# Optimization experiments

Hardware: AMD Instinct MI355X
Metric: run time of the kernel (lower is better)

## Reference

```python
import jax, jax.numpy as jnp
import numpy as np
import math

N_WAY, K_SHOT, Q_QUERY, PRJ_NUM, D = 5, 5, 15, 6, 64


def setup_inputs() -> dict:
    key = jax.random.key(0)
    k1, k2 = jax.random.split(key)
    feat = jax.random.normal(k1, (600, 64, 10, 10), dtype=jnp.float32)
    label = jax.random.randint(k2, (450,), 0, N_WAY)
    scale = jnp.ones((1,), dtype=jnp.float32)
    r = jnp.zeros((2,), dtype=jnp.float32)
    return {"feat": feat, "label": label, "scale": scale, "r": r}


def reference(feat, label, scale, r):
    ns = N_WAY * K_SHOT * PRJ_NUM  # 150 support images
    inv_sqrt_d = 1.0 / math.sqrt(D)
    support_xf = feat[:ns] * inv_sqrt_d
    query_xf = feat[ns:] * inv_sqrt_d
    q, c, h, w = query_xf.shape

    # support: (n_way, k_shot*prj_num*h*w, c)
    support = support_xf.reshape(N_WAY, K_SHOT * PRJ_NUM, c, h * w)
    support = jnp.transpose(support, (0, 1, 3, 2)).reshape(N_WAY, -1, c)
    # query: (q*h*w, c)
    query = jnp.transpose(query_xf.reshape(q, c, h * w), (0, 2, 1)).reshape(q * h * w, c)

    alpha, beta = r[0], r[1]
    reg = support.shape[1] / support.shape[2]
    lam = reg * jnp.exp(alpha)
    rho = jnp.exp(beta)

    # Woodbury / normal-equations path: hat = (S^T S + lam I)^-1 S^T S, per class
    sts = jnp.einsum('nkc,nkd->ncd', support, support)  # (n_way, c, c)
    m = sts + lam * jnp.eye(c, dtype=sts.dtype)[None]
    hat = jnp.linalg.inv(m) @ sts  # (n_way, c, c)

    Q_bar = jnp.einsum('qc,ncd->nqd', query, hat) * rho  # (n_way, q*h*w, c)
    dist = jnp.sum((Q_bar - query[None]) ** 2, axis=2).T  # (q*h*w, n_way)
    neg_l2_dist = -dist.reshape(q, h * w, N_WAY).mean(axis=1)  # (q, n_way)

    y_pred = jax.nn.softmax(neg_l2_dist, axis=1)
    logits = neg_l2_dist * scale[0]
    logp = jax.nn.log_softmax(logits, axis=1)
    loss = -jnp.mean(jnp.take_along_axis(logp, label[:, None], axis=1))
    return y_pred, loss
```

## Files before the change

kernel.cpp:

```cpp
#include <hip/hip_runtime.h>
#include <math.h>


typedef __attribute__((ext_vector_type(8))) short short8;
typedef __attribute__((ext_vector_type(4))) short short4v;
typedef __attribute__((ext_vector_type(4))) float f32x4;

#define NSUP 150
#define NQ 450
#define PIX 100
#define IMG_STRIDE 6400
#define MAGIC 0x5F3D2B1Cu

static __device__ __forceinline__ short bf16r(float x) {
  unsigned u = __builtin_bit_cast(unsigned, x);
  u += 0x7FFFu + ((u >> 16) & 1u);
  return (short)(u >> 16);
}
static __device__ __forceinline__ float b2f(short v) {
  return __builtin_bit_cast(float, ((unsigned)(unsigned short)v) << 16);
}
static __device__ __forceinline__ void st_flag(unsigned* p, unsigned v) {
  __builtin_amdgcn_fence(__ATOMIC_RELEASE, "agent");
  __hip_atomic_store(p, v, __ATOMIC_RELAXED, __HIP_MEMORY_SCOPE_AGENT);
}
static __device__ __forceinline__ void spin_rlx(unsigned* p) {
  int guard = 1 << 22;
  while (__hip_atomic_load(p, __ATOMIC_RELAXED, __HIP_MEMORY_SCOPE_AGENT) != MAGIC
         && --guard) __builtin_amdgcn_s_sleep(2);
}

static __device__ __forceinline__ void gram_accum(const float* __restrict__ f,
                                                  f32x4 acc[4][4], int r, int g) {
  #pragma unroll
  for (int ks = 0; ks < 4; ++ks) {
    short8 frag[4];
    const int kb = ks * 32 + g * 8;
    #pragma unroll
    for (int R = 0; R < 4; ++R) {
      short8 q;
      const float* p = f + (R * 16 + r) * PIX + kb;
      if (ks < 3) {
        float4 lo = *(const float4*)p;
        float4 hi = *(const float4*)(p + 4);
        q[0] = bf16r(lo.x); q[1] = bf16r(lo.y); q[2] = bf16r(lo.z); q[3] = bf16r(lo.w);
        q[4] = bf16r(hi.x); q[5] = bf16r(hi.y); q[6] = bf16r(hi.z); q[7] = bf16r(hi.w);
      } else if (g == 0) {
        float4 lo = *(const float4*)p;
        q[0] = bf16r(lo.x); q[1] = bf16r(lo.y); q[2] = bf16r(lo.z); q[3] = bf16r(lo.w);
        q[4] = 0; q[5] = 0; q[6] = 0; q[7] = 0;
      } else {
        #pragma unroll
        for (int j = 0; j < 8; ++j) q[j] = 0;
      }
      frag[R] = q;
    }
    #pragma unroll
    for (int R = 0; R < 4; ++R)
      #pragma unroll
      for (int C = 0; C < 4; ++C)
        acc[R][C] = __builtin_amdgcn_mfma_f32_16x16x32_bf16(frag[R], frag[C],
                                                            acc[R][C], 0, 0, 0);
  }
}

static __device__ __forceinline__ void mm64q(const short* A, const short* B,
                                             f32x4 t[2][2], int r, int g,
                                             int wr, int wc) {
  #pragma unroll
  for (int ks = 0; ks < 2; ++ks) {
    short8 af[2], bfr[2];
    #pragma unroll
    for (int i = 0; i < 2; ++i) {
      af[i]  = *(const short8*)(A + (wr * 32 + i * 16 + r) * 72 + ks * 32 + g * 8);
      bfr[i] = *(const short8*)(B + (wc * 32 + i * 16 + r) * 72 + ks * 32 + g * 8);
    }
    #pragma unroll
    for (int i = 0; i < 2; ++i)
      #pragma unroll
      for (int j = 0; j < 2; ++j)
        t[i][j] = __builtin_amdgcn_mfma_f32_16x16x32_bf16(af[i], bfr[j],
                                                          t[i][j], 0, 0, 0);
  }
}

#define ZERO_ACC4(t)                                  \
  _Pragma("unroll") for (int R = 0; R < 4; ++R)       \
  _Pragma("unroll") for (int C = 0; C < 4; ++C)       \
  _Pragma("unroll") for (int q = 0; q < 4; ++q) t[R][C][q] = 0.f;

#define ZERO_ACC2(t)                                  \
  _Pragma("unroll") for (int R = 0; R < 2; ++R)       \
  _Pragma("unroll") for (int C = 0; C < 2; ++C)       \
  _Pragma("unroll") for (int q = 0; q < 4; ++q) t[R][C][q] = 0.f;

__global__ __launch_bounds__(256) void k_fused(
    const float* __restrict__ feat, const int* __restrict__ label,
    const float* __restrict__ scale, const float* __restrict__ rvec,
    float* __restrict__ out,
    float* __restrict__ partial,
    unsigned short* __restrict__ Gneg,
    float* __restrict__ blockloss,
    unsigned* __restrict__ gflag,
    unsigned* __restrict__ sflag,
    unsigned* __restrict__ lflag) {
  __shared__ __align__(16) char smem[65536];
  const int b = blockIdx.x, tid = threadIdx.x;
  const int wave = tid >> 6, lane = tid & 63;
  const int r = lane & 15, g = lane >> 4;

  if (b < 30) {
    float (*gbuf)[4096] = (float (*)[4096])smem;
    const int cls = b / 6, jb = b % 6;
    const int ks = wave, kb = ks * 32 + g * 8;
    f32x4 acc[4][4];
    ZERO_ACC4(acc)
    for (int im = 0; im < 5; ++im) {
      const float* f = feat + (size_t)(cls * 30 + jb * 5 + im) * IMG_STRIDE;
      short8 frag[4];
      #pragma unroll
      for (int R = 0; R < 4; ++R) {
        short8 q;
        const float* p = f + (R * 16 + r) * PIX + kb;
        if (ks < 3) {
          float4 lo = *(const float4*)p;
          float4 hi = *(const float4*)(p + 4);
          q[0] = bf16r(lo.x); q[1] = bf16r(lo.y); q[2] = bf16r(lo.z); q[3] = bf16r(lo.w);
          q[4] = bf16r(hi.x); q[5] = bf16r(hi.y); q[6] = bf16r(hi.z); q[7] = bf16r(hi.w);
        } else if (g == 0) {
          float4 lo = *(const float4*)p;
          q[0] = bf16r(lo.x); q[1] = bf16r(lo.y); q[2] = bf16r(lo.z); q[3] = bf16r(lo.w);
          q[4] = 0; q[5] = 0; q[6] = 0; q[7] = 0;
        } else {
          #pragma unroll
          for (int j = 0; j < 8; ++j) q[j] = 0;
        }
        frag[R] = q;
      }
      #pragma unroll
      for (int R = 0; R < 4; ++R)
        #pragma unroll
        for (int C = 0; C < 4; ++C)
          acc[R][C] = __builtin_amdgcn_mfma_f32_16x16x32_bf16(frag[R], frag[C],
                                                              acc[R][C], 0, 0, 0);
    }
    #pragma unroll
    for (int R = 0; R < 4; ++R)
      #pragma unroll
      for (int C = 0; C < 4; ++C)
        #pragma unroll
        for (int q = 0; q < 4; ++q) {
          const int row = R * 16 + g * 4 + q, col = C * 16 + r;
          gbuf[wave][row * 64 + col] = acc[R][C][q];
        }
    __syncthreads();
    float* outp = partial + (size_t)b * 4096;
    for (int c = tid; c < 1024; c += 256) {
      f32x4 s0 = *(const f32x4*)&gbuf[0][4 * c];
      f32x4 s1 = *(const f32x4*)&gbuf[1][4 * c];
      f32x4 s2 = *(const f32x4*)&gbuf[2][4 * c];
      f32x4 s3 = *(const f32x4*)&gbuf[3][4 * c];
      f32x4 s = s0 + s1 + s2 + s3;
      *(float4*)(outp + 4 * c) = *(float4*)&s;
    }
    __syncthreads();
    if (tid == 0) st_flag(&gflag[b], MAGIC);
    if (b >= 5) return;

    float* Ms   = (float*)(smem);
    short* Mb   = (short*)(smem + 16640);
    short* Tb   = (short*)(smem + 25856);
    short* Xa   = (short*)(smem + 35072);
    short* Xc   = (short*)(smem + 44288);
    float* radp = (float*)(smem + 53504);
    float* scal = (float*)(smem + 54528);

    const int n = b;
    const int wr = wave >> 1, wc = wave & 1;
    const float lam = 46.875f * expf(rvec[0]);
    const float rho = expf(rvec[1]);

    if (tid < 6) spin_rlx(&gflag[6 * n + tid]);
    __syncthreads();
    __builtin_amdgcn_fence(__ATOMIC_ACQUIRE, "agent");

    {
      const float* base = partial + (size_t)n * 6 * 4096;
      for (int c = tid; c < 1024; c += 256) {
        float4 s = {0.f, 0.f, 0.f, 0.f};
        #pragma unroll
        for (int p = 0; p < 6; ++p) {
          float4 v = *(const float4*)(base + p * 4096 + 4 * c);
          s.x += v.x; s.y += v.y; s.z += v.z; s.w += v.w;
        }
        const int e = 4 * c, row = e >> 6, col = e & 63;
        Ms[row * 65 + col + 0] = s.x * (1.f / 64.f);
        Ms[row * 65 + col + 1] = s.y * (1.f / 64.f);
        Ms[row * 65 + col + 2] = s.z * (1.f / 64.f);
        Ms[row * 65 + col + 3] = s.w * (1.f / 64.f);
      }
    }
    __syncthreads();
    if (tid < 64) Ms[tid * 65 + tid] += lam;
    __syncthreads();

    {
      const int row = tid & 63, part = tid >> 6;
      float s = 0.f;
      #pragma unroll
      for (int k = 0; k < 16; ++k) s += fabsf(Ms[row * 65 + part * 16 + k]);
      radp[part * 64 + row] = s;
    }
    __syncthreads();
    if (tid < 64) {
      const float diag = Ms[tid * 65 + tid];
      const float rad = radp[tid] + radp[64 + tid] + radp[128 + tid] +
                        radp[192 + tid] - fabsf(diag);
      float lo = diag - rad, hi = diag + rad;
      for (int off = 32; off; off >>= 1) {
        lo = fminf(lo, __shfl_down(lo, off));
        hi = fmaxf(hi, __shfl_down(hi, off));
      }
      if (tid == 0) {
        const float a = fmaxf(lo, lam);
        const float bb = hi;
        const float s = a + bb, d = bb - a;
        scal[0] = s;
        scal[1] = 8.f / (2.f * s * s - d * d);
      }
    }
    __syncthreads();
    const float s0 = scal[0], theta = scal[1];

    for (int e = tid; e < 4096; e += 256) {
      const int i = e >> 6, j = e & 63;
      const float m = Ms[i * 65 + j];
      Mb[i * 72 + j] = bf16r(m);
      Xa[i * 72 + j] = bf16r(theta * (((i == j) ? s0 : 0.f) - m));
    }
    __syncthreads();

    short* x = Xa;
    short* xn = Xc;
    for (int it = 0; it < 2; ++it) {
      {
        f32x4 t[2][2];
        ZERO_ACC2(t)
        mm64q(x, Mb, t, r, g, wr, wc);
        #pragma unroll
        for (int i = 0; i < 2; ++i)
          #pragma unroll
          for (int j = 0; j < 2; ++j)
            #pragma unroll
            for (int q = 0; q < 4; ++q) {
              const int row = wr * 32 + i * 16 + g * 4 + q;
              const int col = wc * 32 + j * 16 + r;
              Tb[row * 72 + col] = bf16r(t[i][j][q]);
            }
      }
      __syncthreads();
      {
        f32x4 t[2][2];
        ZERO_ACC2(t)
        mm64q(Tb, x, t, r, g, wr, wc);
        #pragma unroll
        for (int i = 0; i < 2; ++i)
          #pragma unroll
          for (int j = 0; j < 2; ++j)
            #pragma unroll
            for (int q = 0; q < 4; ++q) {
              const int row = wr * 32 + i * 16 + g * 4 + q;
              const int col = wc * 32 + j * 16 + r;
              const int idx = row * 72 + col;
              xn[idx] = bf16r(2.f * b2f(x[idx]) - t[i][j][q]);
            }
      }
      __syncthreads();
      short* tmp = x; x = xn; xn = tmp;
    }

    for (int e = tid; e < 4096; e += 256) {
      const int i = e >> 6, j = e & 63;
      const float xv = b2f(x[i * 72 + j]);
      Tb[i * 72 + j] = bf16r(((i == j) ? (rho - 1.f) : 0.f) - rho * lam * xv);
    }
    __syncthreads();

    {
      f32x4 t[2][2];
      ZERO_ACC2(t)
      mm64q(Tb, Tb, t, r, g, wr, wc);
      #pragma unroll
      for (int i = 0; i < 2; ++i)
        #pragma unroll
        for (int j = 0; j < 2; ++j)
          #pragma unroll
          for (int q = 0; q < 4; ++q) {
            const int row = wr * 32 + i * 16 + g * 4 + q;
            const int col = wc * 32 + j * 16 + r;
            Gneg[n * 4096 + row * 64 + col] =
                (unsigned short)bf16r(t[i][j][q] * (-0.01f));
          }
    }
    __syncthreads();
    if (tid == 0) st_flag(&sflag[n], MAGIC);
    return;
  }

  const int img = (b - 30) * 4 + wave;
  const bool ok = img < NQ;
  f32x4 acc[4][4];
  ZERO_ACC4(acc)
  if (ok)
    gram_accum(feat + (size_t)(NSUP + img) * IMG_STRIDE, acc, r, g);

  if (tid < 5) spin_rlx(&sflag[tid]);
  __syncthreads();
  __builtin_amdgcn_fence(__ATOMIC_ACQUIRE, "agent");

  unsigned short* Gs = (unsigned short*)smem;
  for (int e = tid; e < 5120; e += 256) {
    const int e4 = e * 4;
    const int nn = e4 >> 12, rem = e4 & 4095, row = rem >> 6, col = rem & 63;
    *(short4v*)&Gs[nn * 4352 + row * 68 + col] = *(const short4v*)&Gneg[e4];
  }
  __syncthreads();

  float myloss = 0.f;
  float nl[5] = {0.f, 0.f, 0.f, 0.f, 0.f};
  if (ok) {
    #pragma unroll
    for (int R = 0; R < 4; ++R)
      #pragma unroll
      for (int C = 0; C < 4; ++C)
        #pragma unroll
        for (int q = 0; q < 4; ++q) {
          const int row = R * 16 + g * 4 + q, col = C * 16 + r;
          const float cv = acc[R][C][q] * (1.f / 64.f);
          const int idx = row * 68 + col;
          #pragma unroll
          for (int nn = 0; nn < 5; ++nn)
            nl[nn] += b2f((short)Gs[nn * 4352 + idx]) * cv;
        }
    #pragma unroll
    for (int nn = 0; nn < 5; ++nn)
      for (int off = 32; off; off >>= 1) nl[nn] += __shfl_down(nl[nn], off);

    if (lane == 0) {
      float mx = nl[0];
      #pragma unroll
      for (int nn = 1; nn < 5; ++nn) mx = fmaxf(mx, nl[nn]);
      float ex[5], se = 0.f;
      #pragma unroll
      for (int nn = 0; nn < 5; ++nn) { ex[nn] = expf(nl[nn] - mx); se += ex[nn]; }
      const float inv = 1.f / se;
      #pragma unroll
      for (int nn = 0; nn < 5; ++nn) out[img * 5 + nn] = ex[nn] * inv;

      const float sc = scale[0];
      float mx2 = nl[0] * sc;
      #pragma unroll
      for (int nn = 1; nn < 5; ++nn) mx2 = fmaxf(mx2, nl[nn] * sc);
      float se2 = 0.f;
      #pragma unroll
      for (int nn = 0; nn < 5; ++nn) se2 += expf(nl[nn] * sc - mx2);
      myloss = mx2 + logf(se2) - nl[label[img]] * sc;
    }
  }

  float* wl = (float*)(smem + 43584);
  if (lane == 0) wl[wave] = ok ? myloss : 0.f;
  __syncthreads();
  if (tid == 0) {
    blockloss[b - 30] = wl[0] + wl[1] + wl[2] + wl[3];
    st_flag(&lflag[b - 30], MAGIC);
  }

  if (b == 30 && wave == 0) {
    for (int i = lane; i < 113; i += 64) spin_rlx(&lflag[i]);
    __builtin_amdgcn_fence(__ATOMIC_ACQUIRE, "agent");
    float s = 0.f;
    for (int i = lane; i < 113; i += 64) s += blockloss[i];
    for (int off = 32; off; off >>= 1) s += __shfl_down(s, off);
    if (lane == 0) out[2250] = s / 450.f;
  }
}

extern "C" void kernel_launch(void* const* d_in, const int* in_sizes, int n_in,
                              void* d_out, int out_size, void* d_ws, size_t ws_size,
                              hipStream_t stream) {
  const float* feat  = (const float*)d_in[0];
  const int*   label = (const int*)d_in[1];
  const float* scale = (const float*)d_in[2];
  const float* rvec  = (const float*)d_in[3];
  float* out = (float*)d_out;

  char* ws = (char*)d_ws;
  float*          partial   = (float*)ws;
  unsigned short* Gneg      = (unsigned short*)(ws + 491520);
  float*          blockloss = (float*)(ws + 532480);
  unsigned*       flags     = (unsigned*)(ws + 532992);
  unsigned* gflag = flags;
  unsigned* sflag = flags + 32;
  unsigned* lflag = flags + 64;

  k_fused<<<dim3(143), dim3(256), 0, stream>>>(feat, label, scale, rvec, out,
                                               partial, Gneg, blockloss,
                                               gflag, sflag, lflag);
}
```

Baseline: 24.40 us.

## Fuse lambda/bf16 staging, unroll Newton-Schulz steps, repad Gs, hoist label/scale loads

Several small changes ship together. The lambda diagonal add and the bf16 conversion of M now happen in the partial-sum reduction loop, which removes one barrier and one pass over shared memory. The two Newton-Schulz iterations are unrolled by hand, and the final residual transform is folded into the last iteration's epilogue, which drops a separate pass and a barrier. The query path loads scale and label before the spin-wait and switches the Gs shared-memory row pitch from 68 to 80 shorts, presumably to change the LDS bank pattern, with loop unroll pragmas added as well. The extra work in the epilogues and the larger LDS footprint could raise register or LDS pressure.

Result: no change. 24.44 us (+0.2%).

```diff
diff --git a/kernel.cpp b/kernel.cpp
--- a/kernel.cpp
+++ b/kernel.cpp
@@ -115,6 +115,7 @@
     const int ks = wave, kb = ks * 32 + g * 8;
     f32x4 acc[4][4];
     ZERO_ACC4(acc)
+    #pragma unroll
     for (int im = 0; im < 5; ++im) {
       const float* f = feat + (size_t)(cls * 30 + jb * 5 + im) * IMG_STRIDE;
       short8 frag[4];
@@ -186,7 +187,9 @@
 
     {
       const float* base = partial + (size_t)n * 6 * 4096;
-      for (int c = tid; c < 1024; c += 256) {
+      #pragma unroll
+      for (int c0 = 0; c0 < 4; ++c0) {
+        const int c = tid + c0 * 256;
         float4 s = {0.f, 0.f, 0.f, 0.f};
         #pragma unroll
         for (int p = 0; p < 6; ++p) {
@@ -194,14 +197,20 @@
           s.x += v.x; s.y += v.y; s.z += v.z; s.w += v.w;
         }
         const int e = 4 * c, row = e >> 6, col = e & 63;
-        Ms[row * 65 + col + 0] = s.x * (1.f / 64.f);
-        Ms[row * 65 + col + 1] = s.y * (1.f / 64.f);
-        Ms[row * 65 + col + 2] = s.z * (1.f / 64.f);
-        Ms[row * 65 + col + 3] = s.w * (1.f / 64.f);
+        const float m0 = s.x * (1.f / 64.f) + ((row == col    ) ? lam : 0.f);
+        const float m1 = s.y * (1.f / 64.f) + ((row == col + 1) ? lam : 0.f);
+        const float m2 = s.z * (1.f / 64.f) + ((row == col + 2) ? lam : 0.f);
+        const float m3 = s.w * (1.f / 64.f) + ((row == col + 3) ? lam : 0.f);
+        Ms[row * 65 + col + 0] = m0;
+        Ms[row * 65 + col + 1] = m1;
+        Ms[row * 65 + col + 2] = m2;
+        Ms[row * 65 + col + 3] = m3;
+        Mb[row * 72 + col + 0] = bf16r(m0);
+        Mb[row * 72 + col + 1] = bf16r(m1);
+        Mb[row * 72 + col + 2] = bf16r(m2);
+        Mb[row * 72 + col + 3] = bf16r(m3);
       }
     }
-    __syncthreads();
-    if (tid < 64) Ms[tid * 65 + tid] += lam;
     __syncthreads();
 
     {
@@ -234,62 +243,81 @@
 
     for (int e = tid; e < 4096; e += 256) {
       const int i = e >> 6, j = e & 63;
-      const float m = Ms[i * 65 + j];
-      Mb[i * 72 + j] = bf16r(m);
-      Xa[i * 72 + j] = bf16r(theta * (((i == j) ? s0 : 0.f) - m));
-    }
-    __syncthreads();
-
-    short* x = Xa;
-    short* xn = Xc;
-    for (int it = 0; it < 2; ++it) {
-      {
-        f32x4 t[2][2];
-        ZERO_ACC2(t)
-        mm64q(x, Mb, t, r, g, wr, wc);
-        #pragma unroll
-        for (int i = 0; i < 2; ++i)
-          #pragma unroll
-          for (int j = 0; j < 2; ++j)
-            #pragma unroll
-            for (int q = 0; q < 4; ++q) {
-              const int row = wr * 32 + i * 16 + g * 4 + q;
-              const int col = wc * 32 + j * 16 + r;
-              Tb[row * 72 + col] = bf16r(t[i][j][q]);
-            }
-      }
-      __syncthreads();
-      {
-        f32x4 t[2][2];
-        ZERO_ACC2(t)
-        mm64q(Tb, x, t, r, g, wr, wc);
-        #pragma unroll
-        for (int i = 0; i < 2; ++i)
-          #pragma unroll
-          for (int j = 0; j < 2; ++j)
-            #pragma unroll
-            for (int q = 0; q < 4; ++q) {
-              const int row = wr * 32 + i * 16 + g * 4 + q;
-              const int col = wc * 32 + j * 16 + r;
-              const int idx = row * 72 + col;
-              xn[idx] = bf16r(2.f * b2f(x[idx]) - t[i][j][q]);
-            }
-      }
-      __syncthreads();
-      short* tmp = x; x = xn; xn = tmp;
-    }
-
-    for (int e = tid; e < 4096; e += 256) {
-      const int i = e >> 6, j = e & 63;
-      const float xv = b2f(x[i * 72 + j]);
-      Tb[i * 72 + j] = bf16r(((i == j) ? (rho - 1.f) : 0.f) - rho * lam * xv);
+      Xa[i * 72 + j] = bf16r(theta * (((i == j) ? s0 : 0.f) - Ms[i * 65 + j]));
     }
     __syncthreads();
 
     {
       f32x4 t[2][2];
       ZERO_ACC2(t)
-      mm64q(Tb, Tb, t, r, g, wr, wc);
+      mm64q(Xa, Mb, t, r, g, wr, wc);
+      #pragma unroll
+      for (int i = 0; i < 2; ++i)
+        #pragma unroll
+        for (int j = 0; j < 2; ++j)
+          #pragma unroll
+          for (int q = 0; q < 4; ++q) {
+            const int row = wr * 32 + i * 16 + g * 4 + q;
+            const int col = wc * 32 + j * 16 + r;
+            Tb[row * 72 + col] = bf16r(t[i][j][q]);
+          }
+    }
+    __syncthreads();
+    {
+      f32x4 t[2][2];
+      ZERO_ACC2(t)
+      mm64q(Tb, Xa, t, r, g, wr, wc);
+      #pragma unroll
+      for (int i = 0; i < 2; ++i)
+        #pragma unroll
+        for (int j = 0; j < 2; ++j)
+          #pragma unroll
+          for (int q = 0; q < 4; ++q) {
+            const int row = wr * 32 + i * 16 + g * 4 + q;
+            const int col = wc * 32 + j * 16 + r;
+            const int idx = row * 72 + col;
+            Xc[idx] = bf16r(2.f * b2f(Xa[idx]) - t[i][j][q]);
+          }
+    }
+    __syncthreads();
+    {
+      f32x4 t[2][2];
+      ZERO_ACC2(t)
+      mm64q(Xc, Mb, t, r, g, wr, wc);
+      #pragma unroll
+      for (int i = 0; i < 2; ++i)
+        #pragma unroll
+        for (int j = 0; j < 2; ++j)
+          #pragma unroll
+          for (int q = 0; q < 4; ++q) {
+            const int row = wr * 32 + i * 16 + g * 4 + q;
+            const int col = wc * 32 + j * 16 + r;
+            Tb[row * 72 + col] = bf16r(t[i][j][q]);
+          }
+    }
+    __syncthreads();
+    {
+      f32x4 t[2][2];
+      ZERO_ACC2(t)
+      mm64q(Tb, Xc, t, r, g, wr, wc);
+      #pragma unroll
+      for (int i = 0; i < 2; ++i)
+        #pragma unroll
+        for (int j = 0; j < 2; ++j)
+          #pragma unroll
+          for (int q = 0; q < 4; ++q) {
+            const int row = wr * 32 + i * 16 + g * 4 + q;
+            const int col = wc * 32 + j * 16 + r;
+            const int idx = row * 72 + col;
+            const float x2 = 2.f * b2f(Xc[idx]) - t[i][j][q];
+            Xa[idx] = bf16r(((row == col) ? (rho - 1.f) : 0.f) - rho * lam * x2);
+          }
+    }
+    __syncthreads();
+    {
+      f32x4 t[2][2];
+      ZERO_ACC2(t)
+      mm64q(Xa, Xa, t, r, g, wr, wc);
       #pragma unroll
       for (int i = 0; i < 2; ++i)
         #pragma unroll
@@ -309,6 +337,8 @@
 
   const int img = (b - 30) * 4 + wave;
   const bool ok = img < NQ;
+  const float sc = scale[0];
+  const int lab = ok ? label[img] : 0;
   f32x4 acc[4][4];
   ZERO_ACC4(acc)
   if (ok)
@@ -322,7 +352,7 @@
   for (int e = tid; e < 5120; e += 256) {
     const int e4 = e * 4;
     const int nn = e4 >> 12, rem = e4 & 4095, row = rem >> 6, col = rem & 63;
-    *(short4v*)&Gs[nn * 4352 + row * 68 + col] = *(const short4v*)&Gneg[e4];
+    *(short4v*)&Gs[nn * 5120 + row * 80 + col] = *(const short4v*)&Gneg[e4];
   }
   __syncthreads();
 
@@ -337,10 +367,10 @@
         for (int q = 0; q < 4; ++q) {
           const int row = R * 16 + g * 4 + q, col = C * 16 + r;
           const float cv = acc[R][C][q] * (1.f / 64.f);
-          const int idx = row * 68 + col;
+          const int idx = row * 80 + col;
           #pragma unroll
           for (int nn = 0; nn < 5; ++nn)
-            nl[nn] += b2f((short)Gs[nn * 4352 + idx]) * cv;
+            nl[nn] += b2f((short)Gs[nn * 5120 + idx]) * cv;
         }
     #pragma unroll
     for (int nn = 0; nn < 5; ++nn)
@@ -357,18 +387,17 @@
       #pragma unroll
       for (int nn = 0; nn < 5; ++nn) out[img * 5 + nn] = ex[nn] * inv;
 
-      const float sc = scale[0];
       float mx2 = nl[0] * sc;
       #pragma unroll
       for (int nn = 1; nn < 5; ++nn) mx2 = fmaxf(mx2, nl[nn] * sc);
       float se2 = 0.f;
       #pragma unroll
       for (int nn = 0; nn < 5; ++nn) se2 += expf(nl[nn] * sc - mx2);
-      myloss = mx2 + logf(se2) - nl[label[img]] * sc;
-    }
-  }
-
-  float* wl = (float*)(smem + 43584);
+      myloss = mx2 + logf(se2) - nl[lab] * sc;
+    }
+  }
+
+  float* wl = (float*)(smem + 51200);
   if (lane == 0) wl[wave] = ok ? myloss : 0.f;
   __syncthreads();
   if (tid == 0) {
```
